# Kernel optimization log

Measured on AMD Instinct MI355X. Metric: run time of the kernel, lower is better.

Reference implementation:

```python
import jax, jax.numpy as jnp
import numpy as np

B, S, D = 4, 4096, 1024

def setup_inputs() -> dict:
    key = jax.random.key(0)
    kx, kq, kk, kv = jax.random.split(key, 4)
    x = jax.random.normal(kx, (B, S, D), dtype=jnp.float32)
    # nn.Linear weights, stored here as [d_in, d_out] so y = x @ W
    scale = 1.0 / np.sqrt(D)
    Wq = jax.random.normal(kq, (D, D), dtype=jnp.float32) * scale
    Wk = jax.random.normal(kk, (D, D), dtype=jnp.float32) * scale
    Wv = jax.random.normal(kv, (D, D), dtype=jnp.float32) * scale
    return {"x": x, "Wq": Wq, "Wk": Wk, "Wv": Wv}

def reference(x, Wq, Wk, Wv):
    b, n, d_in = x.shape
    d_out = Wk.shape[1]
    q = jnp.einsum('bnd,de->bne', x, Wq)
    k = jnp.einsum('bnd,de,->bne', x, Wk, 1.0)  # keys
    v = jnp.einsum('bnd,de->bne', x, Wv)
    # full causal attention: scores scaled by 1/sqrt(d_out) AFTER masking (matches source)
    scores = jnp.einsum('bqe,bke->bqk', q, k)
    causal = jnp.triu(jnp.ones((n, n), dtype=bool), k=1)  # True above diagonal -> masked
    scores = jnp.where(causal[None, :, :], -jnp.inf, scores)
    attn = jax.nn.softmax(scores / jnp.sqrt(jnp.asarray(d_out, scores.dtype)), axis=-1)
    # dropout p=0.0 (eval) -> identity
    return jnp.einsum('bqk,bke->bqe', attn, v)
```

## Files before the change

kernel.cpp:

```cpp
#include <hip/hip_runtime.h>
#include <hip/hip_bf16.h>

#define B_ 4
#define S_ 4096
#define D_ 1024
#define NT_ 32
#define PAIRS_ 528

typedef __attribute__((ext_vector_type(8))) short short8;
typedef __attribute__((ext_vector_type(4))) float f32x4;

__device__ __forceinline__ unsigned short f2bf(float f) {
    union { float f; unsigned u; } v; v.f = f;
    unsigned u = v.u;
    return (unsigned short)((u + 0x7fffu + ((u >> 16) & 1u)) >> 16);
}

__device__ __forceinline__ void gld_lds16(const unsigned short* g, unsigned short* l) {
    __builtin_amdgcn_global_load_lds((const __attribute__((address_space(1))) void*)g,
                                     (__attribute__((address_space(3))) void*)l, 16, 0, 0);
}

#define LGKM0 asm volatile("s_waitcnt lgkmcnt(0)" ::: "memory")
#define VM0   asm volatile("s_waitcnt vmcnt(0)" ::: "memory")
#define VM4   asm volatile("s_waitcnt vmcnt(4)" ::: "memory")
#define VM6   asm volatile("s_waitcnt vmcnt(6)" ::: "memory")
#define BAR   __builtin_amdgcn_s_barrier()
#define SB0   __builtin_amdgcn_sched_barrier(0)

__global__ __launch_bounds__(256) void prep_x(const float* __restrict__ x,
                                              unsigned short* __restrict__ xb) {
    size_t i = ((size_t)blockIdx.x * 256 + threadIdx.x) * 8;
    float4 a = *(const float4*)&x[i];
    float4 b = *(const float4*)&x[i + 4];
    unsigned u0 = (unsigned)f2bf(a.x) | ((unsigned)f2bf(a.y) << 16);
    unsigned u1 = (unsigned)f2bf(a.z) | ((unsigned)f2bf(a.w) << 16);
    unsigned u2 = (unsigned)f2bf(b.x) | ((unsigned)f2bf(b.y) << 16);
    unsigned u3 = (unsigned)f2bf(b.z) | ((unsigned)f2bf(b.w) << 16);
    uint4 val; val.x = u0; val.y = u1; val.z = u2; val.w = u3;
    *(uint4*)&xb[i] = val;
}

__global__ __launch_bounds__(256) void prep_w(const float* __restrict__ Wq,
                                              const float* __restrict__ Wk,
                                              const float* __restrict__ Wv,
                                              unsigned short* __restrict__ Wt) {
    __shared__ float ls[64 * 65];
    const int z = blockIdx.z;
    const float* __restrict__ W = (z == 0) ? Wq : (z == 1) ? Wk : Wv;
    unsigned short* __restrict__ Wtz = Wt + (size_t)z * D_ * D_;
    const int k0 = blockIdx.y * 64, n0 = blockIdx.x * 64;
    const int tid = threadIdx.x;
    #pragma unroll
    for (int i = 0; i < 16; ++i) {
        int lin = i * 256 + tid, r = lin >> 6, c = lin & 63;
        ls[r * 65 + c] = W[(size_t)(k0 + r) * D_ + n0 + c];
    }
    __syncthreads();
    #pragma unroll
    for (int i = 0; i < 16; ++i) {
        int lin = i * 256 + tid, r = lin >> 6, c = lin & 63;
        Wtz[(size_t)(n0 + r) * D_ + k0 + c] = f2bf(ls[c * 65 + r]);
    }
}

__global__ __launch_bounds__(512, 2) void qkv_gemm(
    const unsigned short* __restrict__ xb, const unsigned short* __restrict__ Wt,
    unsigned short* __restrict__ Q, unsigned short* __restrict__ K,
    unsigned short* __restrict__ Vt)
{
    __shared__ __align__(16) unsigned short ls[3 * 16384];

    const int z = blockIdx.z;
    const float scale = (z == 0) ? 0.03125f : 1.0f;

    const int lin = blockIdx.x;
    const int wg = (lin & 7) * 32 + (lin >> 3);
    const int m0 = (wg >> 2) * 256, n0 = (wg & 3) * 256;

    const int tid = threadIdx.x, lane = tid & 63, w = tid >> 6;
    const int wm = w >> 2, wn = w & 3;
    const int quad = lane >> 4, ln = lane & 15;

    const unsigned short* Ab = xb + (size_t)m0 * D_;
    const unsigned short* Bb = Wt + (size_t)z * D_ * D_ + (size_t)n0 * D_;

#define QKV_STAGE(kt, r)                                                          \
    {                                                                             \
        _Pragma("unroll")                                                         \
        for (int i_ = 0; i_ < 2; ++i_) {                                          \
            int g_ = tid + i_ * 512;                                              \
            int row_ = g_ >> 2;                                                   \
            int gs_ = (g_ & 3) ^ ((row_ >> 1) & 3);                               \
            gld_lds16(Ab + (size_t)row_ * D_ + (kt) * 32 + gs_ * 8,               \
                      ls + (r) * 16384 + g_ * 8);                                 \
            gld_lds16(Bb + (size_t)row_ * D_ + (kt) * 32 + gs_ * 8,               \
                      ls + (r) * 16384 + 8192 + g_ * 8);                          \
        }                                                                         \
    }

    f32x4 acc[8][4] = {};

#define QKV_BODY(r)                                                              \
    {                                                                            \
        const unsigned short* As_ = ls + (r) * 16384;                            \
        const unsigned short* Bs_ = As_ + 8192;                                  \
        short8 a_[8], b_[4];                                                     \
        _Pragma("unroll")                                                        \
        for (int mf_ = 0; mf_ < 8; ++mf_) {                                      \
            int row_ = wm * 128 + mf_ * 16 + ln;                                 \
            int g_ = quad ^ ((row_ >> 1) & 3);                                   \
            a_[mf_] = *(const short8*)&As_[row_ * 32 + g_ * 8];                  \
        }                                                                        \
        _Pragma("unroll")                                                        \
        for (int nf_ = 0; nf_ < 4; ++nf_) {                                      \
            int row_ = wn * 64 + nf_ * 16 + ln;                                  \
            int g_ = quad ^ ((row_ >> 1) & 3);                                   \
            b_[nf_] = *(const short8*)&Bs_[row_ * 32 + g_ * 8];                  \
        }                                                                        \
        __builtin_amdgcn_s_setprio(1);                                          \
        _Pragma("unroll")                                                        \
        for (int mf_ = 0; mf_ < 8; ++mf_)                                        \
            _Pragma("unroll")                                                    \
            for (int nf_ = 0; nf_ < 4; ++nf_)                                    \
                acc[mf_][nf_] = __builtin_amdgcn_mfma_f32_16x16x32_bf16(         \
                    a_[mf_], b_[nf_], acc[mf_][nf_], 0, 0, 0);                   \
        __builtin_amdgcn_s_setprio(0);                                          \
    }

#define QKV_STEP(t, r, rn, wcode)                                                \
    {                                                                            \
        if ((wcode) == 0) QKV_STAGE((t) + 2, rn)                                 \
        SB0;                                                                     \
        QKV_BODY(r)                                                              \
        LGKM0; SB0;                                                              \
        if ((wcode) == 0)      { VM4; SB0; BAR; SB0; }                           \
        else if ((wcode) == 1) { VM0; SB0; BAR; SB0; }                           \
    }

    QKV_STAGE(0, 0) QKV_STAGE(1, 1)
    VM4; SB0;
    BAR; SB0;

    #pragma unroll 1
    for (int tb = 0; tb < 30; tb += 3) {
        QKV_STEP(tb,     0, 2, 0)
        QKV_STEP(tb + 1, 1, 0, 0)
        QKV_STEP(tb + 2, 2, 1, 0)
    }
    QKV_STEP(30, 0, 0, 1)
    QKV_STEP(31, 1, 0, 2)

#undef QKV_STAGE
#undef QKV_BODY
#undef QKV_STEP

    if (z != 2) {
        unsigned short* __restrict__ Y = (z == 0) ? Q : K;
        #pragma unroll
        for (int mf = 0; mf < 8; ++mf)
            #pragma unroll
            for (int nf = 0; nf < 4; ++nf)
                #pragma unroll
                for (int rr = 0; rr < 4; ++rr) {
                    int row = m0 + wm * 128 + mf * 16 + quad * 4 + rr;
                    int col = n0 + wn * 64 + nf * 16 + ln;
                    Y[(size_t)row * D_ + col] = f2bf(acc[mf][nf][rr] * scale);
                }
    } else {
        BAR;
        unsigned int* U = (unsigned int*)ls + w * 2080;
        const int b_ = m0 >> 12;
        const int sbase = (m0 & 4095) + wm * 128;
        unsigned int* VtU = (unsigned int*)Vt;
        #pragma unroll
        for (int ch = 0; ch < 2; ++ch) {
            #pragma unroll
            for (int nfl = 0; nfl < 2; ++nfl) {
                int nf = ch * 2 + nfl;
                int el = nfl * 16 + ln;
                #pragma unroll
                for (int mf = 0; mf < 8; ++mf)
                    #pragma unroll
                    for (int pr = 0; pr < 2; ++pr) {
                        unsigned lo = f2bf(acc[mf][nf][2 * pr]);
                        unsigned hi = f2bf(acc[mf][nf][2 * pr + 1]);
                        U[el * 65 + mf * 8 + quad * 2 + pr] = lo | (hi << 16);
                    }
            }
            LGKM0; SB0;
            #pragma unroll 4
            for (int el = 0; el < 32; ++el) {
                unsigned v = U[el * 65 + lane];
                int eg = n0 + wn * 64 + ch * 32 + el;
                VtU[(((size_t)b_ * D_ + eg) * S_ + sbase) / 2 + lane] = v;
            }
            if (ch == 0) { LGKM0; SB0; }
        }
    }
}

__global__ __launch_bounds__(256, 2) void qk_pexp(
    const unsigned short* __restrict__ Q, const unsigned short* __restrict__ K,
    unsigned short* __restrict__ P, float* __restrict__ lpart)
{
    __shared__ __align__(16) unsigned short ls[3 * 12288];
    __shared__ float sml[2][128];

    const int l = blockIdx.x, b = blockIdx.y;
    const int r = l & 7;
    const int s = l >> 3;
    const size_t base = (size_t)b * S_ * D_;
    const int tid = threadIdx.x, lane = tid & 63, w = tid >> 6;
    const int wm = w >> 1, wn = w & 1, quad = lane >> 4, ln = lane & 15;

    if (s < 32) {
        const int qts0 = r, qts1 = 31 - r, qts2 = 8 + r, qts3 = 23 - r;
        int qt = -1, j = 0, rem = s;
        {
            int np;
            np = (qts0 + 1) >> 1; if (rem < np) { qt = qts0; j = rem; } rem -= np;
            np = (qts1 + 1) >> 1; if (qt < 0 && rem < np) { qt = qts1; j = rem; } if (qt < 0) rem -= np;
            np = (qts2 + 1) >> 1; if (qt < 0 && rem < np) { qt = qts2; j = rem; } if (qt < 0) rem -= np;
            if (qt < 0) { qt = qts3; j = rem; }
        }
        const int q0 = qt * 128;
        const int p0 = qt * (qt + 1) / 2 + 2 * j;
        const unsigned short* Qb  = Q + base + (size_t)q0 * D_;
        const unsigned short* Kb2 = K + base + (size_t)(j * 256) * D_;

#define QP_STAGE(c_, r_)                                                          \
    {                                                                             \
        _Pragma("unroll")                                                         \
        for (int i_ = 0; i_ < 2; ++i_) {                                          \
            int g_ = tid + i_ * 256;                                              \
            int row_ = g_ >> 2;                                                   \
            int gs_ = (g_ & 3) ^ ((row_ >> 1) & 3);                               \
            gld_lds16(Qb + (size_t)row_ * D_ + (c_) * 32 + gs_ * 8,               \
                      ls + (r_) * 12288 + g_ * 8);                                \
        }                                                                         \
        _Pragma("unroll")                                                         \
        for (int i_ = 0; i_ < 4; ++i_) {                                          \
            int g_ = tid + i_ * 256;                                              \
            int row_ = g_ >> 2;                                                   \
            int gs_ = (g_ & 3) ^ ((row_ >> 1) & 3);                               \
            gld_lds16(Kb2 + (size_t)row_ * D_ + (c_) * 32 + gs_ * 8,              \
                      ls + (r_) * 12288 + 4096 + g_ * 8);                         \
        }                                                                         \
    }

        f32x4 acc[4][8] = {};

#define QP_BODY(r_)                                                              \
    {                                                                            \
        const unsigned short* As_ = ls + (r_) * 12288;                           \
        const unsigned short* Bs_ = As_ + 4096;                                  \
        short8 a_[4], b_[8];                                                     \
        _Pragma("unroll")                                                        \
        for (int mf_ = 0; mf_ < 4; ++mf_) {                                      \
            int row_ = wm * 64 + mf_ * 16 + ln;                                  \
            int g_ = quad ^ ((row_ >> 1) & 3);                                   \
            a_[mf_] = *(const short8*)&As_[row_ * 32 + g_ * 8];                  \
        }                                                                        \
        _Pragma("unroll")                                                        \
        for (int nf_ = 0; nf_ < 8; ++nf_) {                                      \
            int row_ = wn * 128 + nf_ * 16 + ln;                                 \
            int g_ = quad ^ ((row_ >> 1) & 3);                                   \
            b_[nf_] = *(const short8*)&Bs_[row_ * 32 + g_ * 8];                  \
        }                                                                        \
        __builtin_amdgcn_s_setprio(1);                                          \
        _Pragma("unroll")                                                        \
        for (int mf_ = 0; mf_ < 4; ++mf_)                                        \
            _Pragma("unroll")                                                    \
            for (int nf_ = 0; nf_ < 8; ++nf_)                                    \
                acc[mf_][nf_] = __builtin_amdgcn_mfma_f32_16x16x32_bf16(         \
                    a_[mf_], b_[nf_], acc[mf_][nf_], 0, 0, 0);                   \
        __builtin_amdgcn_s_setprio(0);                                          \
    }

#define QP_STEP(t, r_, rn, wcode)                                                \
    {                                                                            \
        if ((wcode) == 0) QP_STAGE((t) + 2, rn)                                  \
        SB0;                                                                     \
        QP_BODY(r_)                                                              \
        LGKM0; SB0;                                                              \
        if ((wcode) == 0)      { VM6; SB0; BAR; SB0; }                           \
        else if ((wcode) == 1) { VM0; SB0; BAR; SB0; }                           \
    }

        QP_STAGE(0, 0) QP_STAGE(1, 1)
        VM6; SB0;
        BAR; SB0;

        #pragma unroll 1
        for (int tb = 0; tb < 30; tb += 3) {
            QP_STEP(tb,     0, 2, 0)
            QP_STEP(tb + 1, 1, 0, 0)
            QP_STEP(tb + 2, 2, 1, 0)
        }
        QP_STEP(30, 0, 0, 1)
        QP_STEP(31, 1, 0, 2)

#undef QP_STAGE
#undef QP_BODY
#undef QP_STEP

        const bool mt = (2 * j + 1 == qt) && (wn == 1);
        unsigned short* Pt = P + ((size_t)b * PAIRS_ + p0 + wn) * (128 * 128);
        #pragma unroll
        for (int mf = 0; mf < 4; ++mf)
            #pragma unroll
            for (int rr = 0; rr < 4; ++rr) {
                int rowq = wm * 64 + mf * 16 + quad * 4 + rr;
                float lsum = 0.0f;
                #pragma unroll
                for (int nf = 0; nf < 8; ++nf) {
                    int ckey = nf * 16 + ln;
                    float sc = acc[mf][nf][rr];
                    float pe = (mt && ckey > rowq) ? 0.0f : __expf(fminf(sc, 60.0f));
                    Pt[rowq * 128 + ckey] = f2bf(pe);
                    lsum += pe;
                }
                #pragma unroll
                for (int off = 1; off < 16; off <<= 1)
                    lsum += __shfl_xor(lsum, off);
                if (ln == 0) sml[wn][rowq] = lsum;
            }
        __syncthreads();
        if (tid < 128) {
            lpart[((size_t)b * PAIRS_ + p0) * 128 + tid]     = sml[0][tid];
            lpart[((size_t)b * PAIRS_ + p0 + 1) * 128 + tid] = sml[1][tid];
        }
    } else {
        const int qt = (r & 1) ? ((s == 32) ? 31 - r : 23 - r)
                               : ((s == 32) ? r : 8 + r);
        const int q0 = qt * 128;
        const int p = qt * (qt + 1) / 2 + qt;
        const unsigned short* Qb = Q + base + (size_t)q0 * D_;
        const unsigned short* Kb = K + base + (size_t)q0 * D_;

#define QS_STAGE(c_, r_)                                                          \
    {                                                                             \
        _Pragma("unroll")                                                         \
        for (int i_ = 0; i_ < 2; ++i_) {                                          \
            int g_ = tid + i_ * 256;                                              \
            int row_ = g_ >> 2;                                                   \
            int gs_ = (g_ & 3) ^ ((row_ >> 1) & 3);                               \
            gld_lds16(Qb + (size_t)row_ * D_ + (c_) * 32 + gs_ * 8,               \
                      ls + (r_) * 12288 + g_ * 8);                                \
            gld_lds16(Kb + (size_t)row_ * D_ + (c_) * 32 + gs_ * 8,               \
                      ls + (r_) * 12288 + 4096 + g_ * 8);                         \
        }                                                                         \
    }

        f32x4 acc[4][4] = {};

#define QS_BODY(r_)                                                              \
    {                                                                            \
        const unsigned short* As_ = ls + (r_) * 12288;                           \
        const unsigned short* Bs_ = As_ + 4096;                                  \
        short8 a_[4], b_[4];                                                     \
        _Pragma("unroll")                                                        \
        for (int mf_ = 0; mf_ < 4; ++mf_) {                                      \
            int row_ = wm * 64 + mf_ * 16 + ln;                                  \
            int g_ = quad ^ ((row_ >> 1) & 3);                                   \
            a_[mf_] = *(const short8*)&As_[row_ * 32 + g_ * 8];                  \
        }                                                                        \
        _Pragma("unroll")                                                        \
        for (int nf_ = 0; nf_ < 4; ++nf_) {                                      \
            int row_ = wn * 64 + nf_ * 16 + ln;                                  \
            int g_ = quad ^ ((row_ >> 1) & 3);                                   \
            b_[nf_] = *(const short8*)&Bs_[row_ * 32 + g_ * 8];                  \
        }                                                                        \
        __builtin_amdgcn_s_setprio(1);                                          \
        _Pragma("unroll")                                                        \
        for (int mf_ = 0; mf_ < 4; ++mf_)                                        \
            _Pragma("unroll")                                                    \
            for (int nf_ = 0; nf_ < 4; ++nf_)                                    \
                acc[mf_][nf_] = __builtin_amdgcn_mfma_f32_16x16x32_bf16(         \
                    a_[mf_], b_[nf_], acc[mf_][nf_], 0, 0, 0);                   \
        __builtin_amdgcn_s_setprio(0);                                          \
    }

#define QS_STEP(t, r_, rn, wcode)                                                \
    {                                                                            \
        if ((wcode) == 0) QS_STAGE((t) + 2, rn)                                  \
        SB0;                                                                     \
        QS_BODY(r_)                                                              \
        LGKM0; SB0;                                                              \
        if ((wcode) == 0)      { VM4; SB0; BAR; SB0; }                           \
        else if ((wcode) == 1) { VM0; SB0; BAR; SB0; }                           \
    }

        QS_STAGE(0, 0) QS_STAGE(1, 1)
        VM4; SB0;
        BAR; SB0;

        #pragma unroll 1
        for (int tb = 0; tb < 30; tb += 3) {
            QS_STEP(tb,     0, 2, 0)
            QS_STEP(tb + 1, 1, 0, 0)
            QS_STEP(tb + 2, 2, 1, 0)
        }
        QS_STEP(30, 0, 0, 1)
        QS_STEP(31, 1, 0, 2)

#undef QS_STAGE
#undef QS_BODY
#undef QS_STEP

        unsigned short* Pt = P + ((size_t)b * PAIRS_ + p) * (128 * 128);
        #pragma unroll
        for (int mf = 0; mf < 4; ++mf)
            #pragma unroll
            for (int rr = 0; rr < 4; ++rr) {
                int rowq = wm * 64 + mf * 16 + quad * 4 + rr;
                float lsum = 0.0f;
                #pragma unroll
                for (int nf = 0; nf < 4; ++nf) {
                    int ckey = wn * 64 + nf * 16 + ln;
                    float sc = acc[mf][nf][rr];
                    float pe = (ckey > rowq) ? 0.0f : __expf(fminf(sc, 60.0f));
                    Pt[rowq * 128 + ckey] = f2bf(pe);
                    lsum += pe;
                }
                #pragma unroll
                for (int off = 1; off < 16; off <<= 1)
                    lsum += __shfl_xor(lsum, off);
                if (ln == 0) sml[wn][rowq] = lsum;
            }
        __syncthreads();
        if (tid < 128)
            lpart[((size_t)b * PAIRS_ + p) * 128 + tid] = sml[0][tid] + sml[1][tid];
    }
}

__global__ __launch_bounds__(128) void merge_il(const float* __restrict__ lpart,
                                                float* __restrict__ il) {
    const int qt = blockIdx.x, b = blockIdx.y;
    const int row = threadIdx.x;
    const int pbase = qt * (qt + 1) / 2;
    float l = 0.0f;
    for (int kt = 0; kt <= qt; ++kt)
        l += lpart[((size_t)b * PAIRS_ + pbase + kt) * 128 + row];
    il[(size_t)b * S_ + qt * 128 + row] = 1.0f / l;
}

__global__ __launch_bounds__(256, 3) void pv_gemm(
    const unsigned short* __restrict__ P, const unsigned short* __restrict__ Vt,
    const float* __restrict__ il, float* __restrict__ O)
{
    __shared__ __align__(16) unsigned short ls[3 * 8192];

    const int bid = blockIdx.x;
    const int u  = (bid & 7) | ((bid >> 6) << 3);
    const int dt = (bid >> 3) & 7;
    const int pair = u & 15;
    const int b = u >> 4;
    const int d0 = dt * 128;
    const int tid = threadIdx.x, lane = tid & 63, w = tid >> 6;
    const int wm = w >> 1, wn = w & 1, quad = lane >> 4, ln = lane & 15;

    const unsigned short* Vtb = Vt + ((size_t)b * D_ + d0) * S_;

#define PV_STAGE(c_, r_)                                                          \
    {                                                                             \
        const unsigned short* Pt_ = Pbase + (size_t)((c_) >> 2) * (128 * 128);    \
        _Pragma("unroll")                                                         \
        for (int i_ = 0; i_ < 2; ++i_) {                                          \
            int g_ = tid + i_ * 256;                                              \
            int row_ = g_ >> 2;                                                   \
            int gs_ = (g_ & 3) ^ ((row_ >> 1) & 3);                               \
            gld_lds16(Pt_ + (size_t)row_ * 128 + ((c_) & 3) * 32 + gs_ * 8,       \
                      ls + (r_) * 8192 + g_ * 8);                                 \
            gld_lds16(Vtb + (size_t)row_ * S_ + (c_) * 32 + gs_ * 8,              \
                      ls + (r_) * 8192 + 4096 + g_ * 8);                          \
        }                                                                         \
    }

#define PV_BODY(r_)                                                              \
    {                                                                            \
        const unsigned short* As_ = ls + (r_) * 8192;                            \
        const unsigned short* Bs_ = As_ + 4096;                                  \
        short8 a_[4], b_[4];                                                     \
        _Pragma("unroll")                                                        \
        for (int mf_ = 0; mf_ < 4; ++mf_) {                                      \
            int row_ = wm * 64 + mf_ * 16 + ln;                                  \
            int g_ = quad ^ ((row_ >> 1) & 3);                                   \
            a_[mf_] = *(const short8*)&As_[row_ * 32 + g_ * 8];                  \
        }                                                                        \
        _Pragma("unroll")                                                        \
        for (int nf_ = 0; nf_ < 4; ++nf_) {                                      \
            int row_ = wn * 64 + nf_ * 16 + ln;                                  \
            int g_ = quad ^ ((row_ >> 1) & 3);                                   \
            b_[nf_] = *(const short8*)&Bs_[row_ * 32 + g_ * 8];                  \
        }                                                                        \
        __builtin_amdgcn_s_setprio(1);                                          \
        _Pragma("unroll")                                                        \
        for (int mf_ = 0; mf_ < 4; ++mf_)                                        \
            _Pragma("unroll")                                                    \
            for (int nf_ = 0; nf_ < 4; ++nf_)                                    \
                acc[mf_][nf_] = __builtin_amdgcn_mfma_f32_16x16x32_bf16(         \
                    a_[mf_], b_[nf_], acc[mf_][nf_], 0, 0, 0);                   \
        __builtin_amdgcn_s_setprio(0);                                          \
    }

    #pragma unroll 1
    for (int half = 0; half < 2; ++half) {
        const int qt = half ? pair : (31 - pair);
        const int q0 = qt * 128;
        const int pbase = qt * (qt + 1) / 2;
        const int nst = 4 * (qt + 1);
        const unsigned short* Pbase = P + ((size_t)b * PAIRS_ + pbase) * (128 * 128);

        f32x4 acc[4][4] = {};

        if (half) { BAR; SB0; }
        PV_STAGE(0, 0) PV_STAGE(1, 1)
        VM4; SB0;
        BAR; SB0;

        #pragma unroll 1
        for (int t = 0; t < nst; ++t) {
            const int r_ = t % 3;
            if (t + 2 < nst) { const int rn_ = (t + 2) % 3; PV_STAGE(t + 2, rn_) }
            SB0;
            PV_BODY(r_)
            LGKM0; SB0;
            if (t + 2 < nst)      { VM4; SB0; }
            else if (t + 1 < nst) { VM0; SB0; }
            if (t + 1 < nst) { BAR; SB0; }
        }

        #pragma unroll
        for (int mf = 0; mf < 4; ++mf) {
            float ilv[4];
            #pragma unroll
            for (int rr = 0; rr < 4; ++rr)
                ilv[rr] = il[(size_t)b * S_ + q0 + wm * 64 + mf * 16 + quad * 4 + rr];
            #pragma unroll
            for (int nf = 0; nf < 4; ++nf)
                #pragma unroll
                for (int rr = 0; rr < 4; ++rr) {
                    int rowq = q0 + wm * 64 + mf * 16 + quad * 4 + rr;
                    int col = d0 + wn * 64 + nf * 16 + ln;
                    O[((size_t)b * S_ + rowq) * D_ + col] = acc[mf][nf][rr] * ilv[rr];
                }
        }
    }
#undef PV_STAGE
#undef PV_BODY
}

extern "C" void kernel_launch(void* const* d_in, const int* in_sizes, int n_in,
                              void* d_out, int out_size, void* d_ws, size_t ws_size,
                              hipStream_t stream) {
    const float* x  = (const float*)d_in[0];
    const float* Wq = (const float*)d_in[1];
    const float* Wk = (const float*)d_in[2];
    const float* Wv = (const float*)d_in[3];

    const size_t nQ = (size_t)B_ * S_ * D_;
    const size_t nP = (size_t)B_ * PAIRS_ * 128 * 128;

    unsigned short* P  = (unsigned short*)d_ws;
    unsigned short* xb = P;
    unsigned short* Q  = P + nP;
    unsigned short* K  = Q + nQ;
    unsigned short* Vt = K + nQ;
    unsigned short* Wt = Vt + nQ;
    float* lpart = (float*)(Wt + (size_t)3 * D_ * D_);
    float* il    = lpart + (size_t)B_ * PAIRS_ * 128;
    float* O = (float*)d_out;

    hipLaunchKernelGGL(prep_x, dim3(8192), dim3(256), 0, stream, x, xb);
    hipLaunchKernelGGL(prep_w, dim3(16, 16, 3), dim3(256), 0, stream, Wq, Wk, Wv, Wt);
    hipLaunchKernelGGL(qkv_gemm, dim3(256, 1, 3), dim3(512), 0, stream, xb, Wt, Q, K, Vt);
    hipLaunchKernelGGL(qk_pexp, dim3(272, B_), dim3(256), 0, stream, Q, K, P, lpart);
    hipLaunchKernelGGL(merge_il, dim3(NT_, B_), dim3(128), 0, stream, lpart, il);
    hipLaunchKernelGGL(pv_gemm, dim3(512), dim3(256), 0, stream, P, Vt, il, O);
}
```

Measured before the change: 405.2 us.

## Restructure QKV GEMM to BK=64 double buffer and PV to register-staged loads

The QKV projection GEMM moves from a triple-buffered K-step of 32 to a double-buffered K-step of 64 with an 8-way XOR swizzle. That halves the number of barriers and iterations, and A fragments are loaded in two halves to cap register use. The PV kernel stops staging P through LDS and loads P fragments straight into registers. V tiles go through registers into a double-buffered LDS with ping-pong prefetch. The QKV change uses more LDS (128KB), which may lower occupancy, and the PV change adds register pressure and exposed global latency.

```diff
diff --git a/kernel.cpp b/kernel.cpp
--- a/kernel.cpp
+++ b/kernel.cpp
@@ -69,7 +69,9 @@
     unsigned short* __restrict__ Q, unsigned short* __restrict__ K,
     unsigned short* __restrict__ Vt)
 {
-    __shared__ __align__(16) unsigned short ls[3 * 16384];
+    __shared__ __align__(16) unsigned short ls[65536];
+    unsigned short* const lsA = ls;
+    unsigned short* const lsB = ls + 32768;
 
     const int z = blockIdx.z;
     const float scale = (z == 0) ? 0.03125f : 1.0f;
@@ -85,75 +87,95 @@
     const unsigned short* Ab = xb + (size_t)m0 * D_;
     const unsigned short* Bb = Wt + (size_t)z * D_ * D_ + (size_t)n0 * D_;
 
-#define QKV_STAGE(kt, r)                                                          \
-    {                                                                             \
-        _Pragma("unroll")                                                         \
-        for (int i_ = 0; i_ < 2; ++i_) {                                          \
-            int g_ = tid + i_ * 512;                                              \
-            int row_ = g_ >> 2;                                                   \
-            int gs_ = (g_ & 3) ^ ((row_ >> 1) & 3);                               \
-            gld_lds16(Ab + (size_t)row_ * D_ + (kt) * 32 + gs_ * 8,               \
-                      ls + (r) * 16384 + g_ * 8);                                 \
-            gld_lds16(Bb + (size_t)row_ * D_ + (kt) * 32 + gs_ * 8,               \
-                      ls + (r) * 16384 + 8192 + g_ * 8);                          \
-        }                                                                         \
-    }
-
+#define STAGE_HALF(gbase, ldsbase)                                              \
+    {                                                                           \
+        _Pragma("unroll")                                                       \
+        for (int i_ = 0; i_ < 2; ++i_) {                                        \
+            int g_ = tid + i_ * 512;                                            \
+            int r_ = g_ >> 3;                                                   \
+            int cg_ = (g_ & 7) ^ (r_ & 7);                                      \
+            gld_lds16((gbase) + (size_t)r_ * D_ + cg_ * 8, (ldsbase) + g_ * 8); \
+        }                                                                       \
+    }
+#define STAGE(kt, h)                                                                   \
+    {                                                                                  \
+        if ((h) < 2) { STAGE_HALF(Ab + (size_t)((h) * 128) * D_ + (kt) * 64,           \
+                                  &lsA[(((kt) & 1) * 2 + (h)) * 8192]) }               \
+        else         { STAGE_HALF(Bb + (size_t)(((h) - 2) * 128) * D_ + (kt) * 64,     \
+                                  &lsB[(((kt) & 1) * 2 + ((h) - 2)) * 8192]) }         \
+    }
+
+    const unsigned short* As;
+    const unsigned short* Bs;
+    short8 a[4][2], b[4][2];
     f32x4 acc[8][4] = {};
 
-#define QKV_BODY(r)                                                              \
-    {                                                                            \
-        const unsigned short* As_ = ls + (r) * 16384;                            \
-        const unsigned short* Bs_ = As_ + 8192;                                  \
-        short8 a_[8], b_[4];                                                     \
-        _Pragma("unroll")                                                        \
-        for (int mf_ = 0; mf_ < 8; ++mf_) {                                      \
-            int row_ = wm * 128 + mf_ * 16 + ln;                                 \
-            int g_ = quad ^ ((row_ >> 1) & 3);                                   \
-            a_[mf_] = *(const short8*)&As_[row_ * 32 + g_ * 8];                  \
-        }                                                                        \
-        _Pragma("unroll")                                                        \
-        for (int nf_ = 0; nf_ < 4; ++nf_) {                                      \
-            int row_ = wn * 64 + nf_ * 16 + ln;                                  \
-            int g_ = quad ^ ((row_ >> 1) & 3);                                   \
-            b_[nf_] = *(const short8*)&Bs_[row_ * 32 + g_ * 8];                  \
-        }                                                                        \
-        __builtin_amdgcn_s_setprio(1);                                          \
-        _Pragma("unroll")                                                        \
-        for (int mf_ = 0; mf_ < 8; ++mf_)                                        \
-            _Pragma("unroll")                                                    \
-            for (int nf_ = 0; nf_ < 4; ++nf_)                                    \
-                acc[mf_][nf_] = __builtin_amdgcn_mfma_f32_16x16x32_bf16(         \
-                    a_[mf_], b_[nf_], acc[mf_][nf_], 0, 0, 0);                   \
-        __builtin_amdgcn_s_setprio(0);                                          \
-    }
-
-#define QKV_STEP(t, r, rn, wcode)                                                \
-    {                                                                            \
-        if ((wcode) == 0) QKV_STAGE((t) + 2, rn)                                 \
-        SB0;                                                                     \
-        QKV_BODY(r)                                                              \
-        LGKM0; SB0;                                                              \
-        if ((wcode) == 0)      { VM4; SB0; BAR; SB0; }                           \
-        else if ((wcode) == 1) { VM0; SB0; BAR; SB0; }                           \
-    }
-
-    QKV_STAGE(0, 0) QKV_STAGE(1, 1)
-    VM4; SB0;
+#define LDA(mh)                                                                        \
+    {                                                                                  \
+        _Pragma("unroll")                                                              \
+        for (int mf_ = 0; mf_ < 4; ++mf_) {                                            \
+            _Pragma("unroll")                                                          \
+            for (int ks_ = 0; ks_ < 2; ++ks_) {                                        \
+                int r_ = wm * 128 + ((mh) * 4 + mf_) * 16 + ln;                        \
+                int cg_ = ks_ * 4 + quad;                                              \
+                a[mf_][ks_] = *(const short8*)&As[r_ * 64 + ((cg_ ^ (r_ & 7)) << 3)];  \
+            }                                                                          \
+        }                                                                              \
+    }
+#define LDB_ALL                                                                        \
+    {                                                                                  \
+        _Pragma("unroll")                                                              \
+        for (int nf_ = 0; nf_ < 4; ++nf_) {                                            \
+            _Pragma("unroll")                                                          \
+            for (int ks_ = 0; ks_ < 2; ++ks_) {                                        \
+                int r_ = wn * 64 + nf_ * 16 + ln;                                      \
+                int cg_ = ks_ * 4 + quad;                                              \
+                b[nf_][ks_] = *(const short8*)&Bs[r_ * 64 + ((cg_ ^ (r_ & 7)) << 3)];  \
+            }                                                                          \
+        }                                                                              \
+    }
+#define MM_H(mh)                                                                       \
+    {                                                                                  \
+        __builtin_amdgcn_s_setprio(1);                                                 \
+        _Pragma("unroll")                                                              \
+        for (int mf_ = 0; mf_ < 4; ++mf_)                                              \
+            _Pragma("unroll")                                                          \
+            for (int nf_ = 0; nf_ < 4; ++nf_)                                          \
+                _Pragma("unroll")                                                      \
+                for (int ks_ = 0; ks_ < 2; ++ks_)                                      \
+                    acc[(mh) * 4 + mf_][nf_] =                                         \
+                        __builtin_amdgcn_mfma_f32_16x16x32_bf16(                       \
+                            a[mf_][ks_], b[nf_][ks_],                                  \
+                            acc[(mh) * 4 + mf_][nf_], 0, 0, 0);                        \
+        __builtin_amdgcn_s_setprio(0);                                                 \
+    }
+
+    STAGE(0, 0) STAGE(0, 1) STAGE(0, 2) STAGE(0, 3)
+    VM0; SB0;
     BAR; SB0;
 
-    #pragma unroll 1
-    for (int tb = 0; tb < 30; tb += 3) {
-        QKV_STEP(tb,     0, 2, 0)
-        QKV_STEP(tb + 1, 1, 0, 0)
-        QKV_STEP(tb + 2, 2, 1, 0)
-    }
-    QKV_STEP(30, 0, 0, 1)
-    QKV_STEP(31, 1, 0, 2)
-
-#undef QKV_STAGE
-#undef QKV_BODY
-#undef QKV_STEP
+    #pragma unroll 2
+    for (int t = 0; t < 16; ++t) {
+        As = lsA + (t & 1) * 16384;
+        Bs = lsB + (t & 1) * 16384;
+        if (t < 15) { STAGE(t + 1, 0) STAGE(t + 1, 1) STAGE(t + 1, 2) STAGE(t + 1, 3) }
+        SB0;
+        LDA(0) LDB_ALL
+        MM_H(0)
+        LDA(1)
+        MM_H(1)
+        LGKM0; SB0;
+        if (t < 15) {
+            VM0; SB0;
+            BAR; SB0;
+        }
+    }
+
+#undef STAGE_HALF
+#undef STAGE
+#undef LDA
+#undef LDB_ALL
+#undef MM_H
 
     if (z != 2) {
         unsigned short* __restrict__ Y = (z == 0) ? Q : K;
@@ -450,7 +472,7 @@
     const unsigned short* __restrict__ P, const unsigned short* __restrict__ Vt,
     const float* __restrict__ il, float* __restrict__ O)
 {
-    __shared__ __align__(16) unsigned short ls[3 * 8192];
+    __shared__ __align__(16) unsigned short lsB[2 * 4096];
 
     const int bid = blockIdx.x;
     const int u  = (bid & 7) | ((bid >> 6) << 3);
@@ -463,47 +485,63 @@
 
     const unsigned short* Vtb = Vt + ((size_t)b * D_ + d0) * S_;
 
-#define PV_STAGE(c_, r_)                                                          \
+#define PV_LOADB(c_, arr)                                                         \
     {                                                                             \
-        const unsigned short* Pt_ = Pbase + (size_t)((c_) >> 2) * (128 * 128);    \
         _Pragma("unroll")                                                         \
         for (int i_ = 0; i_ < 2; ++i_) {                                          \
             int g_ = tid + i_ * 256;                                              \
             int row_ = g_ >> 2;                                                   \
-            int gs_ = (g_ & 3) ^ ((row_ >> 1) & 3);                               \
-            gld_lds16(Pt_ + (size_t)row_ * 128 + ((c_) & 3) * 32 + gs_ * 8,       \
-                      ls + (r_) * 8192 + g_ * 8);                                 \
-            gld_lds16(Vtb + (size_t)row_ * S_ + (c_) * 32 + gs_ * 8,              \
-                      ls + (r_) * 8192 + 4096 + g_ * 8);                          \
+            arr[i_] = *(const short8*)&Vtb[(size_t)row_ * S_ + (c_) * 32 +        \
+                                           (g_ & 3) * 8];                         \
         }                                                                         \
     }
-
-#define PV_BODY(r_)                                                              \
-    {                                                                            \
-        const unsigned short* As_ = ls + (r_) * 8192;                            \
-        const unsigned short* Bs_ = As_ + 4096;                                  \
-        short8 a_[4], b_[4];                                                     \
-        _Pragma("unroll")                                                        \
-        for (int mf_ = 0; mf_ < 4; ++mf_) {                                      \
-            int row_ = wm * 64 + mf_ * 16 + ln;                                  \
-            int g_ = quad ^ ((row_ >> 1) & 3);                                   \
-            a_[mf_] = *(const short8*)&As_[row_ * 32 + g_ * 8];                  \
-        }                                                                        \
-        _Pragma("unroll")                                                        \
-        for (int nf_ = 0; nf_ < 4; ++nf_) {                                      \
-            int row_ = wn * 64 + nf_ * 16 + ln;                                  \
-            int g_ = quad ^ ((row_ >> 1) & 3);                                   \
-            b_[nf_] = *(const short8*)&Bs_[row_ * 32 + g_ * 8];                  \
-        }                                                                        \
-        __builtin_amdgcn_s_setprio(1);                                          \
-        _Pragma("unroll")                                                        \
-        for (int mf_ = 0; mf_ < 4; ++mf_)                                        \
-            _Pragma("unroll")                                                    \
-            for (int nf_ = 0; nf_ < 4; ++nf_)                                    \
-                acc[mf_][nf_] = __builtin_amdgcn_mfma_f32_16x16x32_bf16(         \
-                    a_[mf_], b_[nf_], acc[mf_][nf_], 0, 0, 0);                   \
-        __builtin_amdgcn_s_setprio(0);                                          \
-    }
+#define PV_WRITEB(arr, sl_)                                                       \
+    {                                                                             \
+        _Pragma("unroll")                                                         \
+        for (int i_ = 0; i_ < 2; ++i_) {                                          \
+            int g_ = tid + i_ * 256;                                              \
+            int row_ = g_ >> 2;                                                   \
+            int sw_ = (g_ & 3) ^ ((row_ >> 1) & 3);                               \
+            *(short8*)&lsB[(sl_) * 4096 + row_ * 32 + sw_ * 8] = arr[i_];         \
+        }                                                                         \
+    }
+#define PV_LOADA(t_, arr)                                                         \
+    {                                                                             \
+        const unsigned short* Pt_ = Pbase + (size_t)((t_) >> 2) * (128 * 128) +   \
+                                    ((t_) & 3) * 32;                              \
+        _Pragma("unroll")                                                         \
+        for (int mf_ = 0; mf_ < 4; ++mf_)                                         \
+            arr[mf_] = *(const short8*)&Pt_[(wm * 64 + mf_ * 16 + ln) * 128 +     \
+                                            quad * 8];                            \
+    }
+#define PV_BODY(sl_, arr)                                                         \
+    {                                                                             \
+        short8 bf_[4];                                                            \
+        _Pragma("unroll")                                                         \
+        for (int nf_ = 0; nf_ < 4; ++nf_) {                                       \
+            int row_ = wn * 64 + nf_ * 16 + ln;                                   \
+            int g_ = quad ^ ((row_ >> 1) & 3);                                    \
+            bf_[nf_] = *(const short8*)&lsB[(sl_) * 4096 + row_ * 32 + g_ * 8];   \
+        }                                                                         \
+        __builtin_amdgcn_s_setprio(1);                                           \
+        _Pragma("unroll")                                                         \
+        for (int mf_ = 0; mf_ < 4; ++mf_)                                         \
+            _Pragma("unroll")                                                     \
+            for (int nf_ = 0; nf_ < 4; ++nf_)                                     \
+                acc[mf_][nf_] = __builtin_amdgcn_mfma_f32_16x16x32_bf16(          \
+                    arr[mf_], bf_[nf_], acc[mf_][nf_], 0, 0, 0);                  \
+        __builtin_amdgcn_s_setprio(0);                                           \
+    }
+#define PV_ITER(t_, acur, anxt, brfree, brwr, sl_)                                \
+    {                                                                             \
+        if ((t_) + 2 < nst) PV_LOADB((t_) + 2, brfree)                            \
+        if ((t_) + 1 < nst) PV_LOADA((t_) + 1, anxt)                              \
+        SB0;                                                                      \
+        PV_BODY(sl_, acur)                                                        \
+        if ((t_) + 1 < nst) { PV_WRITEB(brwr, (sl_) ^ 1) LGKM0; BAR; SB0; }       \
+    }
+
+    short8 a0[4], a1[4], br0[2], br1[2];
 
     #pragma unroll 1
     for (int half = 0; half < 2; ++half) {
@@ -515,21 +553,17 @@
 
         f32x4 acc[4][4] = {};
 
-        if (half) { BAR; SB0; }
-        PV_STAGE(0, 0) PV_STAGE(1, 1)
-        VM4; SB0;
-        BAR; SB0;
+        PV_LOADB(0, br0)
+        PV_LOADB(1, br1)
+        PV_LOADA(0, a0)
+        if (half) { BAR; }
+        PV_WRITEB(br0, 0)
+        LGKM0; BAR; SB0;
 
         #pragma unroll 1
-        for (int t = 0; t < nst; ++t) {
-            const int r_ = t % 3;
-            if (t + 2 < nst) { const int rn_ = (t + 2) % 3; PV_STAGE(t + 2, rn_) }
-            SB0;
-            PV_BODY(r_)
-            LGKM0; SB0;
-            if (t + 2 < nst)      { VM4; SB0; }
-            else if (t + 1 < nst) { VM0; SB0; }
-            if (t + 1 < nst) { BAR; SB0; }
+        for (int t = 0; t < nst; t += 2) {
+            PV_ITER(t,     a0, a1, br0, br1, 0)
+            PV_ITER(t + 1, a1, a0, br1, br0, 1)
         }
 
         #pragma unroll
@@ -548,8 +582,11 @@
                 }
         }
     }
-#undef PV_STAGE
+#undef PV_LOADB
+#undef PV_WRITEB
+#undef PV_LOADA
 #undef PV_BODY
+#undef PV_ITER
 }
 
 extern "C" void kernel_launch(void* const* d_in, const int* in_sizes, int n_in,
```

Result: slower. 494.5 us (+22.0%).
